# Kernel optimization log

Hardware: AMD Instinct MI355X
Metric: run time of the kernel (lower is better)

The kernel has to match this reference:

```python
import math
import jax, jax.numpy as jnp
import numpy as np


def conv2d(x, w, b, pad=0, dil=1):
    # x: [B, Cin, H, W], w: [Cout, Cin, kh, kw] (OIHW)
    y = jax.lax.conv_general_dilated(
        x, w, window_strides=(1, 1),
        padding=[(pad, pad), (pad, pad)],
        rhs_dilation=(dil, dil),
        dimension_numbers=('NCHW', 'OIHW', 'NCHW'))
    return y + b[None, :, None, None]


def setup_inputs() -> dict:
    key = jax.random.key(0)
    ks = jax.random.split(key, 8)
    B, C, H, W = 2, 64, 96, 96
    inner = 64 // 18  # = 3, as in the torch module
    n_dil = 3
    s = 0.1
    x = jax.random.normal(ks[0], (B, C, H, W), jnp.float32)
    w_red = jax.random.normal(ks[1], (inner, C, 1, 1), jnp.float32) * s
    b_red = jax.random.normal(ks[2], (inner,), jnp.float32) * s
    w_dil = jax.random.normal(ks[3], (n_dil, inner, inner, 3, 3), jnp.float32) * s
    b_dil = jax.random.normal(ks[4], (n_dil, inner), jnp.float32) * s
    w_fuse = jax.random.normal(ks[5], (C, inner * n_dil * 6, 1, 1), jnp.float32) * s
    b_fuse = jax.random.normal(ks[6], (C,), jnp.float32) * s
    return {"x": x, "w_red": w_red, "b_red": b_red, "w_dil": w_dil,
            "b_dil": b_dil, "w_fuse": w_fuse, "b_fuse": b_fuse}


def _c4_transforms(x):
    # identity, flip-W, flip-H, rot90 k=1,2,3 over spatial dims
    return [x,
            jnp.flip(x, axis=-1),
            jnp.flip(x, axis=-2),
            jnp.rot90(x, 1, axes=(2, 3)),
            jnp.rot90(x, 2, axes=(2, 3)),
            jnp.rot90(x, 3, axes=(2, 3))]


def reference(x, w_red, b_red, w_dil, b_dil, w_fuse, b_fuse):
    dilations = (1, 2, 3)
    residual_scale = 0.2
    B, C, H, W = x.shape
    x_red = conv2d(x, w_red, b_red)                    # [B, inner, H, W]
    tfs = _c4_transforms(x_red)
    feats = []
    for i, d in enumerate(dilations):
        co = conv2d(x_red, w_dil[i], b_dil[i], pad=d, dil=d)
        for tf in tfs:
            feats.append(co * tf)
    cat = jnp.concatenate(feats, axis=1)               # [B, inner*18, H, W]
    fused = conv2d(cat, w_fuse, b_fuse)                # [B, C, H, W]
    tokens = fused.reshape(B, C, H * W).transpose(0, 2, 1)  # [B, N, C]
    # Chunked attention in the original is mathematically full self-attention
    scores = jnp.einsum('bnc,bmc->bnm', tokens, tokens) / math.sqrt(C)
    attn = jax.nn.softmax(scores, axis=-1)
    out = jnp.einsum('bnm,bmc->bnc', attn, tokens)     # [B, N, C]
    out = out.transpose(0, 2, 1).reshape(B, C, H, W)
    return x + residual_scale * out
```

## Files before the change

kernel.cpp:

```cpp
#include <hip/hip_runtime.h>

#define HW    96
#define NPIX  9216
#define NCH   64
#define INNER 3
#define NDIL  3
#define BB    2
#define TOTPIX (BB * NPIX)
#define NT32  (NPIX / 32)

typedef __attribute__((ext_vector_type(8))) short short8;
typedef __attribute__((ext_vector_type(8))) unsigned short ushort8;
typedef __attribute__((ext_vector_type(4))) float f32x4;

__device__ __forceinline__ ushort f2bf_rne(float f) {
    unsigned u = __float_as_uint(f);
    u += 0x7fffu + ((u >> 16) & 1u);
    return (ushort)(u >> 16);
}
__device__ __forceinline__ float bf2f(ushort u) {
    return __uint_as_float((unsigned)u << 16);
}
__device__ __forceinline__ unsigned pack_bf(float lo, float hi) {
    return __builtin_amdgcn_perm(__float_as_uint(hi), __float_as_uint(lo), 0x07060302u);
}

__global__ void k_reduce(const float* __restrict__ x, const float* __restrict__ w_red,
                         const float* __restrict__ b_red, float* __restrict__ xred) {
    int pix = blockIdx.x * blockDim.x + threadIdx.x;
    if (pix >= TOTPIX) return;
    int b = pix / NPIX, n = pix % NPIX;
    float a0 = b_red[0], a1 = b_red[1], a2 = b_red[2];
    const float* xb = x + (size_t)b * NCH * NPIX + n;
    #pragma unroll
    for (int c = 0; c < NCH; ++c) {
        float xv = xb[(size_t)c * NPIX];
        a0 = fmaf(w_red[0 * NCH + c], xv, a0);
        a1 = fmaf(w_red[1 * NCH + c], xv, a1);
        a2 = fmaf(w_red[2 * NCH + c], xv, a2);
    }
    float* xr = xred + (size_t)b * INNER * NPIX + n;
    xr[0 * NPIX] = a0; xr[1 * NPIX] = a1; xr[2 * NPIX] = a2;
}

__global__ __launch_bounds__(256) void
k_feat(const float* __restrict__ xred, const float* __restrict__ w_dil,
       const float* __restrict__ b_dil, ushort* __restrict__ FT) {
    int gid = blockIdx.x * 256 + threadIdx.x;
    int i3 = gid / TOTPIX;
    int pix = gid - i3 * TOTPIX;
    int b = pix / NPIX, n = pix % NPIX;
    int h = n / HW, w = n % HW;
    const float* xr = xred + (size_t)b * INNER * NPIX;
    int d = i3 + 1;

    float co[3] = {b_dil[i3 * 3 + 0], b_dil[i3 * 3 + 1], b_dil[i3 * 3 + 2]};
    #pragma unroll
    for (int ci = 0; ci < 3; ++ci) {
        const float* xo = xr + ci * NPIX;
        #pragma unroll
        for (int kh = 0; kh < 3; ++kh) {
            int hh = h + (kh - 1) * d;
            #pragma unroll
            for (int kw = 0; kw < 3; ++kw) {
                int ww = w + (kw - 1) * d;
                float v = ((unsigned)hh < HW && (unsigned)ww < HW) ? xo[hh * HW + ww] : 0.f;
                #pragma unroll
                for (int o = 0; o < 3; ++o)
                    co[o] = fmaf(w_dil[(9 * i3 + 3 * o + ci) * 9 + kh * 3 + kw], v, co[o]);
            }
        }
    }

    float tf[6][3];
    #pragma unroll
    for (int o = 0; o < 3; ++o) {
        const float* xo = xr + o * NPIX;
        tf[0][o] = xo[h * HW + w];
        tf[1][o] = xo[h * HW + (HW - 1 - w)];
        tf[2][o] = xo[(HW - 1 - h) * HW + w];
        tf[3][o] = xo[w * HW + (HW - 1 - h)];
        tf[4][o] = xo[(HW - 1 - h) * HW + (HW - 1 - w)];
        tf[5][o] = xo[(HW - 1 - w) * HW + h];
    }

    #pragma unroll
    for (int t = 0; t < 6; ++t)
        #pragma unroll
        for (int o = 0; o < 3; ++o) {
            int j = i3 * 18 + t * 3 + o;
            FT[(size_t)j * TOTPIX + pix] = f2bf_rne(co[o] * tf[t][o]);
        }
}

__global__ __launch_bounds__(256) void
k_fuse(const ushort* __restrict__ FT, const float* __restrict__ w_fuse,
       const float* __restrict__ b_fuse, ushort* __restrict__ tok,
       ushort* __restrict__ tokTt) {
    __shared__ ushort wpad[64 * 72];
    __shared__ float  bsh[64];
    __shared__ ushort tile[64 * 72];

    int tid = threadIdx.x;
    for (int i = tid; i < 64 * 64; i += 256) {
        int c = i >> 6, j = i & 63;
        wpad[c * 72 + j] = (j < 54) ? f2bf_rne(w_fuse[c * 54 + j]) : (ushort)0;
    }
    if (tid < 64) bsh[tid] = b_fuse[tid];
    __syncthreads();

    int wv = tid >> 6, lane = tid & 63, quad = lane >> 4, l15 = lane & 15;
    int px0 = blockIdx.x * 64;

    short8 af[4][2];
    #pragma unroll
    for (int m = 0; m < 4; ++m)
        #pragma unroll
        for (int kc = 0; kc < 2; ++kc)
            af[m][kc] = *(const short8*)&wpad[(16 * m + l15) * 72 + quad * 8 + 32 * kc];

    f32x4 acc[4];
    #pragma unroll
    for (int m = 0; m < 4; ++m) acc[m] = (f32x4){0.f, 0.f, 0.f, 0.f};

    int px = px0 + wv * 16 + l15;
    #pragma unroll
    for (int kc = 0; kc < 2; ++kc) {
        short8 bf;
        #pragma unroll
        for (int jj = 0; jj < 8; ++jj)
            bf[jj] = (short)FT[(size_t)(quad * 8 + jj + 32 * kc) * TOTPIX + px];
        #pragma unroll
        for (int m = 0; m < 4; ++m)
            acc[m] = __builtin_amdgcn_mfma_f32_16x16x32_bf16(af[m][kc], bf, acc[m], 0, 0, 0);
    }

    #pragma unroll
    for (int m = 0; m < 4; ++m)
        #pragma unroll
        for (int r = 0; r < 4; ++r) {
            int c = 16 * m + quad * 4 + r;
            tile[c * 72 + wv * 16 + l15] = f2bf_rne(acc[m][r] + bsh[c]);
        }
    __syncthreads();

    int b0 = px0 / NPIX, n0 = px0 % NPIX;
    {
        int lp = tid >> 2, part = tid & 3;
        ushort row[16];
        #pragma unroll
        for (int k = 0; k < 16; ++k) row[k] = tile[(part * 16 + k) * 72 + lp];
        ushort* dst = tok + ((size_t)b0 * NPIX + n0 + lp) * NCH + part * 16;
        *(ushort8*)&dst[0] = *(const ushort8*)&row[0];
        *(ushort8*)&dst[8] = *(const ushort8*)&row[8];
    }
    {
        int c = tid >> 2, seg = tid & 3;
        int n = n0 + seg * 16;
        size_t base = (((size_t)b0 * NT32 + (n >> 5)) * 64 + c) * 32 + (n & 31);
        *(ushort8*)&tokTt[base]     = *(const ushort8*)&tile[c * 72 + seg * 16];
        *(ushort8*)&tokTt[base + 8] = *(const ushort8*)&tile[c * 72 + seg * 16 + 8];
    }
}

__global__ __launch_bounds__(256, 4) void
k_attn(const ushort* __restrict__ tok, const ushort* __restrict__ tokTt,
       float* __restrict__ pl, ushort* __restrict__ pacc, int P, int KP) {
    __shared__ ushort pt[4][32 * 40];
    __shared__ ushort ldsK[2][32 * 80];
    __shared__ ushort ldsV[2][64 * 40];

    const int QW = NPIX / 128;
    int bid = blockIdx.x;
    int qc = bid % QW; int rest = bid / QW;
    int p = rest % P;  int b = rest / P;
    int tid = threadIdx.x;
    int wv = tid >> 6, lane = tid & 63;
    int quad = lane >> 4, l15 = lane & 15;

    const ushort* tb  = tok + (size_t)b * NPIX * NCH;
    const ushort* tvb = tokTt + (size_t)b * NT32 * (64 * 32);
    int qwave = qc * 128 + wv * 32;

    int sk_off = (tid >> 3) * 80 + (tid & 7) * 8;
    int sv_off = (tid >> 2) * 40 + (tid & 3) * 8;

    short8 qf[2][2];
    const float scale = 0.125f * 1.44269504088896340736f;
    #pragma unroll
    for (int n = 0; n < 2; ++n) {
        const ushort* qr = tb + (size_t)(qwave + 16 * n + l15) * NCH + quad * 8;
        #pragma unroll
        for (int kc = 0; kc < 2; ++kc) {
            ushort8 raw = *(const ushort8*)(qr + 32 * kc);
            short8 f;
            #pragma unroll
            for (int e = 0; e < 8; ++e) f[e] = (short)f2bf_rne(bf2f(raw[e]) * scale);
            qf[n][kc] = f;
        }
    }

    f32x4 O[4][2];
    #pragma unroll
    for (int m = 0; m < 4; ++m)
        #pragma unroll
        for (int n = 0; n < 2; ++n) O[m][n] = (f32x4){0.f, 0.f, 0.f, 0.f};
    float lrun[2] = {0.f, 0.f};

    const float FM = 16.0f;
    int k0 = p * KP;
    ushort* ptw = &pt[wv][0];
    int nt = KP / 32;

    {
        ushort8 gK = *(const ushort8*)(tb + (size_t)k0 * NCH + tid * 8);
        ushort8 gV = *(const ushort8*)(tvb + ((size_t)(k0 >> 5)) * 2048 + tid * 8);
        *(ushort8*)&ldsK[0][sk_off] = gK;
        *(ushort8*)&ldsV[0][sv_off] = gV;
    }
    __syncthreads();

    for (int t = 0; t < nt; ++t) {
        int cur = t & 1;
        int kbase = k0 + t * 32;
        bool pre = (t + 1 < nt);

        ushort8 nK, nV;
        if (pre) {
            nK = *(const ushort8*)(tb + (size_t)(kbase + 32) * NCH + tid * 8);
            nV = *(const ushort8*)(tvb + ((size_t)((kbase + 32) >> 5)) * 2048 + tid * 8);
        }

        short8 kd[4];
        #pragma unroll
        for (int m2 = 0; m2 < 2; ++m2)
            #pragma unroll
            for (int kc = 0; kc < 2; ++kc)
                kd[2 * m2 + kc] = *(const short8*)&ldsK[cur][(16 * m2 + l15) * 80 +
                                                            quad * 8 + 32 * kc];

        f32x4 S[2][2];
        #pragma unroll
        for (int m = 0; m < 2; ++m)
            #pragma unroll
            for (int n = 0; n < 2; ++n) S[m][n] = (f32x4){0.f, 0.f, 0.f, 0.f};

        __builtin_amdgcn_s_setprio(1);
        #pragma unroll
        for (int m2 = 0; m2 < 2; ++m2)
            #pragma unroll
            for (int cc = 0; cc < 2; ++cc)
                #pragma unroll
                for (int n = 0; n < 2; ++n)
                    S[m2][n] = __builtin_amdgcn_mfma_f32_16x16x32_bf16(kd[2 * m2 + cc],
                                                                       qf[n][cc], S[m2][n],
                                                                       0, 0, 0);
        __builtin_amdgcn_s_setprio(0);

        if (pre) {
            *(ushort8*)&ldsK[cur ^ 1][sk_off] = nK;
            *(ushort8*)&ldsV[cur ^ 1][sv_off] = nV;
        }

        short8 vf[4];
        #pragma unroll
        for (int mc = 0; mc < 4; ++mc)
            vf[mc] = *(const short8*)&ldsV[cur][(16 * mc + l15) * 40 + quad * 8];

        #pragma unroll
        for (int n = 0; n < 2; ++n) {
            int q = 16 * n + l15;
            #pragma unroll
            for (int m2 = 0; m2 < 2; ++m2) {
                float p0 = __builtin_amdgcn_exp2f(S[m2][n][0] - FM);
                float p1 = __builtin_amdgcn_exp2f(S[m2][n][1] - FM);
                float p2 = __builtin_amdgcn_exp2f(S[m2][n][2] - FM);
                float p3 = __builtin_amdgcn_exp2f(S[m2][n][3] - FM);
                lrun[n] += (p0 + p1) + (p2 + p3);
                uint2 wd = make_uint2(pack_bf(p0, p1), pack_bf(p2, p3));
                *(uint2*)&ptw[q * 40 + m2 * 16 + quad * 4] = wd;
            }
        }

        __builtin_amdgcn_s_setprio(1);
        #pragma unroll
        for (int n = 0; n < 2; ++n) {
            short8 bfr = *(const short8*)&ptw[(16 * n + l15) * 40 + quad * 8];
            #pragma unroll
            for (int mc = 0; mc < 4; ++mc)
                O[mc][n] = __builtin_amdgcn_mfma_f32_16x16x32_bf16(vf[mc], bfr,
                                                                   O[mc][n], 0, 0, 0);
        }
        __builtin_amdgcn_s_setprio(0);

        __syncthreads();
    }

    #pragma unroll
    for (int n = 0; n < 2; ++n) {
        lrun[n] += __shfl_xor(lrun[n], 16, 64);
        lrun[n] += __shfl_xor(lrun[n], 32, 64);
    }
    size_t bp = (size_t)b * P + p;
    if (quad == 0) {
        #pragma unroll
        for (int n = 0; n < 2; ++n)
            pl[bp * NPIX + qwave + 16 * n + l15] = lrun[n];
    }
    #pragma unroll
    for (int n = 0; n < 2; ++n) {
        int qg = qwave + 16 * n + l15;
        #pragma unroll
        for (int m = 0; m < 4; ++m) {
            #pragma unroll
            for (int r = 0; r < 4; ++r) {
                int c = 16 * m + quad * 4 + r;
                pacc[(bp * NCH + c) * NPIX + qg] = f2bf_rne(O[m][n][r]);
            }
        }
    }
}

__global__ void k_norm(const float* __restrict__ pl, float* __restrict__ linv, int P) {
    int idx = blockIdx.x * blockDim.x + threadIdx.x;
    if (idx >= TOTPIX) return;
    int b = idx / NPIX, n = idx % NPIX;
    float L = 0.f;
    for (int p = 0; p < P; ++p) L += pl[((size_t)b * P + p) * NPIX + n];
    linv[idx] = 0.2f / L;
}

__global__ void k_combine(const float* __restrict__ x, const float* __restrict__ linv,
                          const ushort* __restrict__ pacc, float* __restrict__ out,
                          int P) {
    int gid = blockIdx.x * blockDim.x + threadIdx.x;
    if (gid >= BB * NCH * (NPIX / 8)) return;
    int seg = gid % (NPIX / 8);
    int bc  = gid / (NPIX / 8);
    int b = bc / NCH;
    int n0 = seg * 8;
    float o[8] = {0.f, 0.f, 0.f, 0.f, 0.f, 0.f, 0.f, 0.f};
    for (int p = 0; p < P; ++p) {
        ushort8 t = *(const ushort8*)(pacc +
            (((size_t)b * P + p) * NCH + (bc % NCH)) * NPIX + n0);
        #pragma unroll
        for (int e = 0; e < 8; ++e) o[e] += bf2f(t[e]);
    }
    const float* lv = linv + (size_t)b * NPIX + n0;
    const float* xb = x + (size_t)bc * NPIX + n0;
    float* ob = out + (size_t)bc * NPIX + n0;
    #pragma unroll
    for (int e = 0; e < 8; ++e)
        ob[e] = fmaf(lv[e], o[e], xb[e]);
}

extern "C" void kernel_launch(void* const* d_in, const int* in_sizes, int n_in,
                              void* d_out, int out_size, void* d_ws, size_t ws_size,
                              hipStream_t stream) {
    const float* x      = (const float*)d_in[0];
    const float* w_red  = (const float*)d_in[1];
    const float* b_red  = (const float*)d_in[2];
    const float* w_dil  = (const float*)d_in[3];
    const float* b_dil  = (const float*)d_in[4];
    const float* w_fuse = (const float*)d_in[5];
    const float* b_fuse = (const float*)d_in[6];
    float* out = (float*)d_out;

    const size_t XRED_N = (size_t)BB * INNER * NPIX;
    const size_t FT_N   = (size_t)64 * TOTPIX;
    const size_t TOK_N  = (size_t)BB * NPIX * NCH;
    const size_t HEAD_B = XRED_N * 4 + (FT_N + 2 * TOK_N) * 2 + TOTPIX * 4;
    int P = 0;
    const int cands[5] = {16, 8, 4, 2, 1};
    for (int ci = 0; ci < 5; ++ci) {
        int cp = cands[ci];
        size_t need = HEAD_B + (size_t)BB * cp * NPIX * (4 + NCH * 2);
        if (ws_size >= need) { P = cp; break; }
    }
    if (P == 0) return;

    float*  xred  = (float*)d_ws;
    ushort* FT    = (ushort*)(xred + XRED_N);
    ushort* tok   = FT + FT_N;
    ushort* tokTt = tok + TOK_N;
    float*  pl    = (float*)(tokTt + TOK_N);
    float*  linv  = pl + (size_t)BB * P * NPIX;
    ushort* pacc  = (ushort*)(linv + TOTPIX);

    k_reduce <<<(TOTPIX + 255) / 256, 256, 0, stream>>>(x, w_red, b_red, xred);
    k_feat   <<<3 * TOTPIX / 256, 256, 0, stream>>>(xred, w_dil, b_dil, FT);
    k_fuse   <<<TOTPIX / 64, 256, 0, stream>>>(FT, w_fuse, b_fuse, tok, tokTt);
    k_attn   <<<BB * P * (NPIX / 128), 256, 0, stream>>>(tok, tokTt, pl, pacc,
                                                         P, NPIX / P);
    k_norm   <<<(TOTPIX + 255) / 256, 256, 0, stream>>>(pl, linv, P);
    k_combine<<<(BB * NCH * (NPIX / 8) + 255) / 256, 256, 0, stream>>>(x, linv, pacc,
                                                                       out, P);
}
```

Baseline: 150.6 us.

## Keep softmax probabilities in registers by permuting V layout in LDS

Removes the per-wave LDS staging buffer for the exponentiated scores. The probabilities are packed straight from the QK MFMA accumulators into the B operand of the PV MFMA. To make this register layout match, V is written to LDS with a permuted key ordering, split into two 8-byte stores per thread. The K row stride in LDS is also reduced from 80 to 72. This cuts LDS write/read traffic and latency in the inner loop, at the cost of narrower V stores and possible bank-conflict changes.

```diff
diff --git a/kernel.cpp b/kernel.cpp
--- a/kernel.cpp
+++ b/kernel.cpp
@@ -12,6 +12,7 @@
 typedef __attribute__((ext_vector_type(8))) short short8;
 typedef __attribute__((ext_vector_type(8))) unsigned short ushort8;
 typedef __attribute__((ext_vector_type(4))) float f32x4;
+typedef __attribute__((ext_vector_type(4))) unsigned int uint32x4;
 
 __device__ __forceinline__ ushort f2bf_rne(float f) {
     unsigned u = __float_as_uint(f);
@@ -166,8 +167,7 @@
 __global__ __launch_bounds__(256, 4) void
 k_attn(const ushort* __restrict__ tok, const ushort* __restrict__ tokTt,
        float* __restrict__ pl, ushort* __restrict__ pacc, int P, int KP) {
-    __shared__ ushort pt[4][32 * 40];
-    __shared__ ushort ldsK[2][32 * 80];
+    __shared__ ushort ldsK[2][32 * 72];
     __shared__ ushort ldsV[2][64 * 40];
 
     const int QW = NPIX / 128;
@@ -182,8 +182,10 @@
     const ushort* tvb = tokTt + (size_t)b * NT32 * (64 * 32);
     int qwave = qc * 128 + wv * 32;
 
-    int sk_off = (tid >> 3) * 80 + (tid & 7) * 8;
-    int sv_off = (tid >> 2) * 40 + (tid & 3) * 8;
+    int sk_off = (tid >> 3) * 72 + (tid & 7) * 8;
+    int svj = tid & 3;
+    int sv_b0 = (tid >> 2) * 40 + 8 * ((2 * svj) & 3) + 4 * (svj >> 1);
+    int sv_b1 = (tid >> 2) * 40 + 8 * ((2 * svj + 1) & 3) + 4 * (svj >> 1);
 
     short8 qf[2][2];
     const float scale = 0.125f * 1.44269504088896340736f;
@@ -209,14 +211,15 @@
 
     const float FM = 16.0f;
     int k0 = p * KP;
-    ushort* ptw = &pt[wv][0];
     int nt = KP / 32;
 
     {
         ushort8 gK = *(const ushort8*)(tb + (size_t)k0 * NCH + tid * 8);
         ushort8 gV = *(const ushort8*)(tvb + ((size_t)(k0 >> 5)) * 2048 + tid * 8);
         *(ushort8*)&ldsK[0][sk_off] = gK;
-        *(ushort8*)&ldsV[0][sv_off] = gV;
+        uint32x4 v4 = *(uint32x4*)&gV;
+        *(uint2*)&ldsV[0][sv_b0] = make_uint2(v4.x, v4.y);
+        *(uint2*)&ldsV[0][sv_b1] = make_uint2(v4.z, v4.w);
     }
     __syncthreads();
 
@@ -236,7 +239,7 @@
         for (int m2 = 0; m2 < 2; ++m2)
             #pragma unroll
             for (int kc = 0; kc < 2; ++kc)
-                kd[2 * m2 + kc] = *(const short8*)&ldsK[cur][(16 * m2 + l15) * 80 +
+                kd[2 * m2 + kc] = *(const short8*)&ldsK[cur][(16 * m2 + l15) * 72 +
                                                             quad * 8 + 32 * kc];
 
         f32x4 S[2][2];
@@ -259,7 +262,9 @@
 
         if (pre) {
             *(ushort8*)&ldsK[cur ^ 1][sk_off] = nK;
-            *(ushort8*)&ldsV[cur ^ 1][sv_off] = nV;
+            uint32x4 v4 = *(uint32x4*)&nV;
+            *(uint2*)&ldsV[cur ^ 1][sv_b0] = make_uint2(v4.x, v4.y);
+            *(uint2*)&ldsV[cur ^ 1][sv_b1] = make_uint2(v4.z, v4.w);
         }
 
         short8 vf[4];
@@ -269,29 +274,27 @@
 
         #pragma unroll
         for (int n = 0; n < 2; ++n) {
-            int q = 16 * n + l15;
-            #pragma unroll
-            for (int m2 = 0; m2 < 2; ++m2) {
-                float p0 = __builtin_amdgcn_exp2f(S[m2][n][0] - FM);
-                float p1 = __builtin_amdgcn_exp2f(S[m2][n][1] - FM);
-                float p2 = __builtin_amdgcn_exp2f(S[m2][n][2] - FM);
-                float p3 = __builtin_amdgcn_exp2f(S[m2][n][3] - FM);
-                lrun[n] += (p0 + p1) + (p2 + p3);
-                uint2 wd = make_uint2(pack_bf(p0, p1), pack_bf(p2, p3));
-                *(uint2*)&ptw[q * 40 + m2 * 16 + quad * 4] = wd;
-            }
-        }
-
-        __builtin_amdgcn_s_setprio(1);
-        #pragma unroll
-        for (int n = 0; n < 2; ++n) {
-            short8 bfr = *(const short8*)&ptw[(16 * n + l15) * 40 + quad * 8];
+            float e00 = __builtin_amdgcn_exp2f(S[0][n][0] - FM);
+            float e01 = __builtin_amdgcn_exp2f(S[0][n][1] - FM);
+            float e02 = __builtin_amdgcn_exp2f(S[0][n][2] - FM);
+            float e03 = __builtin_amdgcn_exp2f(S[0][n][3] - FM);
+            float e10 = __builtin_amdgcn_exp2f(S[1][n][0] - FM);
+            float e11 = __builtin_amdgcn_exp2f(S[1][n][1] - FM);
+            float e12 = __builtin_amdgcn_exp2f(S[1][n][2] - FM);
+            float e13 = __builtin_amdgcn_exp2f(S[1][n][3] - FM);
+            lrun[n] += ((e00 + e01) + (e02 + e03)) + ((e10 + e11) + (e12 + e13));
+            uint32x4 w;
+            w.x = pack_bf(e00, e01); w.y = pack_bf(e02, e03);
+            w.z = pack_bf(e10, e11); w.w = pack_bf(e12, e13);
+            short8 bfr = *(short8*)&w;
+
+            __builtin_amdgcn_s_setprio(1);
             #pragma unroll
             for (int mc = 0; mc < 4; ++mc)
                 O[mc][n] = __builtin_amdgcn_mfma_f32_16x16x32_bf16(vf[mc], bfr,
                                                                    O[mc][n], 0, 0, 0);
-        }
-        __builtin_amdgcn_s_setprio(0);
+            __builtin_amdgcn_s_setprio(0);
+        }
 
         __syncthreads();
     }
```

After: 149.1 us. About the same (-1.0%).
